# Kernel optimization log

Hardware: AMD Instinct MI355X
Metric: run time of the kernel (lower is better)

Reference implementation:

```python
import jax, jax.numpy as jnp
import numpy as np

T, N, E, F_IN, H_GNN, H_OUT, RH, G, C = 8, 10000, 160000, 128, 128, 128, 128, 32, 10


def gcn_layer(x, src, dst, W, b):
    # PyG GCNConv: h = D^-1/2 (A+I) D^-1/2 (x W) + b, self-loops added, edge weight 1
    h = x @ W  # [N, H]
    ones = jnp.ones((E,), h.dtype)
    deg = jax.ops.segment_sum(ones, dst, num_segments=N) + 1.0  # +1 for self-loop
    dinv = jax.lax.rsqrt(deg)
    coef = dinv[src] * dinv[dst]  # [E]
    agg = jax.ops.segment_sum(h[src] * coef[:, None], dst, num_segments=N)
    agg = agg + h * (dinv * dinv)[:, None]  # self-loop term
    return agg + b


def snapshot_encode(x, edge_index, batch, W1, b1, W2, b2):
    src, dst = edge_index[0], edge_index[1]
    h = jax.nn.relu(gcn_layer(x, src, dst, W1, b1))
    h = jax.nn.relu(gcn_layer(h, src, dst, W2, b2))
    sums = jax.ops.segment_sum(h, batch, num_segments=G)  # global_mean_pool
    cnts = jax.ops.segment_sum(jnp.ones((N,), h.dtype), batch, num_segments=G)
    return sums / jnp.maximum(cnts, 1.0)[:, None]  # [G, H_OUT]


def gru_layer(seq, Wih, Whh, bih, bhh):
    # seq: [T, G, in]; torch nn.GRU cell equations
    H = Whh.shape[1]

    def step(h, xt):
        gi = xt @ Wih.T + bih
        gh = h @ Whh.T + bhh
        ir, iz, inn = jnp.split(gi, 3, axis=-1)
        hr, hz, hn = jnp.split(gh, 3, axis=-1)
        r = jax.nn.sigmoid(ir + hr)
        z = jax.nn.sigmoid(iz + hz)
        n = jnp.tanh(inn + r * hn)
        h_new = (1.0 - z) * n + z * h
        return h_new, h_new

    h0 = jnp.zeros((seq.shape[1], H), seq.dtype)
    hT, outs = jax.lax.scan(step, h0, seq)
    return outs, hT


def setup_inputs() -> dict:
    key = jax.random.key(0)
    ks = jax.random.split(key, 20)
    s = 0.05
    inp = {
        "x": jax.random.normal(ks[0], (T, N, F_IN), jnp.float32),
        "edge_index": jax.random.randint(ks[1], (T, 2, E), 0, N),
        "batch": jax.random.randint(ks[2], (T, N), 0, G),
        "W1": jax.random.normal(ks[3], (F_IN, H_GNN), jnp.float32) * s,
        "b1": jnp.zeros((H_GNN,), jnp.float32),
        "W2": jax.random.normal(ks[4], (H_GNN, H_OUT), jnp.float32) * s,
        "b2": jnp.zeros((H_OUT,), jnp.float32),
        "Wih0": jax.random.normal(ks[5], (3 * RH, H_OUT), jnp.float32) * s,
        "Whh0": jax.random.normal(ks[6], (3 * RH, RH), jnp.float32) * s,
        "bih0": jnp.zeros((3 * RH,), jnp.float32),
        "bhh0": jnp.zeros((3 * RH,), jnp.float32),
        "Wih1": jax.random.normal(ks[7], (3 * RH, RH), jnp.float32) * s,
        "Whh1": jax.random.normal(ks[8], (3 * RH, RH), jnp.float32) * s,
        "bih1": jnp.zeros((3 * RH,), jnp.float32),
        "bhh1": jnp.zeros((3 * RH,), jnp.float32),
        "Wc": jax.random.normal(ks[9], (C, RH), jnp.float32) * s,
        "bc": jnp.zeros((C,), jnp.float32),
    }
    return inp


def reference(x, edge_index, batch, W1, b1, W2, b2, Wih0, Whh0, bih0, bhh0,
              Wih1, Whh1, bih1, bhh1, Wc, bc):
    # per-snapshot GNN encode, vmapped over T snapshots -> [T, G, H_OUT]
    emb = jax.vmap(snapshot_encode, in_axes=(0, 0, 0, None, None, None, None))(
        x, edge_index, batch, W1, b1, W2, b2)
    outs, _ = gru_layer(emb, Wih0, Whh0, bih0, bhh0)
    _, hT = gru_layer(outs, Wih1, Whh1, bih1, bhh1)  # h_n[-1]: last layer final state
    return hT @ Wc.T + bc  # [G, C]
```

## Files before the change

kernel.cpp:

```cpp
#include <hip/hip_runtime.h>

#define T_ 8
#define N_ 10000
#define E_ 160000
#define G_ 32
#define C_ 10
#define F_ 128

typedef _Float16 f16;
typedef _Float16 f16x2 __attribute__((ext_vector_type(2)));
typedef _Float16 f16x4 __attribute__((ext_vector_type(4)));
typedef _Float16 f16x8 __attribute__((ext_vector_type(8)));
typedef float floatx4 __attribute__((ext_vector_type(4)));

static constexpr int NSL = 16;
static constexpr int SLICE = E_ / NSL;

static constexpr size_t OFF_XH    = 0;
static constexpr size_t OFF_A1    = 20480000;
static constexpr size_t OFF_H1    = 40960000;
static constexpr size_t OFF_REC   = 61440000;
static constexpr size_t OFF_CNT   = 66560000;
static constexpr size_t OFF_DINV  = 71680000;
static constexpr size_t OFF_RP    = 72000000;
static constexpr size_t OFF_CNTG  = 72320032;
static constexpr size_t OFF_BRP   = 72321056;
static constexpr size_t OFF_WP    = 72322112;
static constexpr size_t OFF_BLIST = 72387648;
static constexpr size_t OFF_GPACK = 72707648;
static constexpr size_t OFF_PART  = 73100864;

__device__ __forceinline__ float sig_fast(float x) {
  return __builtin_amdgcn_rcpf(1.0f + __builtin_amdgcn_exp2f(-1.4426950408889634f * x));
}
__device__ __forceinline__ float tanh_fast(float x) {
  return 1.0f - 2.0f * __builtin_amdgcn_rcpf(1.0f + __builtin_amdgcn_exp2f(2.8853900817779268f * x));
}

__global__ __launch_bounds__(1024) void prep0_kernel(const int* __restrict__ ei,
                                                     const int* __restrict__ batch,
                                                     int* __restrict__ cnt,
                                                     int* __restrict__ cntG,
                                                     const float* __restrict__ W1,
                                                     const float* __restrict__ W2,
                                                     f16* __restrict__ Wp,
                                                     const float* __restrict__ A0,
                                                     const float* __restrict__ A1,
                                                     const float* __restrict__ A2,
                                                     const float* __restrict__ A3,
                                                     f16* __restrict__ gp) {
  __shared__ int hL[N_];
  __shared__ int cL[G_];
  int b = blockIdx.x, tid = threadIdx.x;
  if (b >= 128) {
    int idx = (b - 128) * 1024 + tid;
    if (idx < 32768) {
      const float* W = (idx < 16384) ? W1 : W2;
      int l = idx & 16383;
      int j = l & 7, lane = (l >> 3) & 63, ct = (l >> 9) & 7, kc = (l >> 12) & 3;
      int k = kc * 32 + ((lane >> 4) & 3) * 8 + j;
      int n = ct * 16 + (lane & 15);
      Wp[idx] = (f16)W[k * 128 + n];
    } else {
      int gidx = idx - 32768;
      int mat = gidx / 49152, l = gidx - mat * 49152;
      int j = l & 7, lane = (l >> 3) & 63, kc = (l >> 9) & 3, nt = l >> 11;
      int k = kc * 32 + ((lane >> 4) & 3) * 8 + j;
      int u = nt * 16 + (lane & 15);
      const float* W = (mat == 0) ? A0 : (mat == 1) ? A1 : (mat == 2) ? A2 : A3;
      gp[gidx] = (f16)W[u * 128 + k];
    }
    return;
  }
  int t = b & 7, s = b >> 3;
  for (int i = tid; i < N_; i += 1024) hL[i] = 0;
  if (tid < G_) cL[tid] = 0;
  __syncthreads();
  const int* dstp = ei + (size_t)t * 2 * E_ + E_ + s * SLICE;
  for (int e4 = tid; e4 < SLICE / 4; e4 += 1024) {
    int4 d = *(const int4*)(dstp + e4 * 4);
    atomicAdd(&hL[d.x], 1); atomicAdd(&hL[d.y], 1);
    atomicAdd(&hL[d.z], 1); atomicAdd(&hL[d.w], 1);
  }
  if (s == 0)
    for (int n = tid; n < N_; n += 1024) atomicAdd(&cL[batch[t * N_ + n]], 1);
  __syncthreads();
  int* cp = cnt + ((size_t)t * NSL + s) * N_;
  for (int i = tid; i < N_; i += 1024) cp[i] = hL[i];
  if (s == 0 && tid < G_) cntG[t * G_ + tid] = cL[tid];
}

__global__ __launch_bounds__(1024) void scan_kernel(int* __restrict__ cnt,
                                                    int* __restrict__ rp,
                                                    float* __restrict__ dinv,
                                                    const int* __restrict__ cntG,
                                                    int* __restrict__ brp) {
  __shared__ int wsum[16];
  __shared__ int carry;
  int t = blockIdx.x, tid = threadIdx.x, lane = tid & 63, wid = tid >> 6;
  if (t == 8) {
    int v = (tid < 256) ? cntG[tid] : 0;
    for (int ofs = 1; ofs < 64; ofs <<= 1) {
      int u = __shfl_up(v, ofs);
      if (lane >= ofs) v += u;
    }
    if (lane == 63 && wid < 4) wsum[wid] = v;
    __syncthreads();
    if (tid < 256) {
      int base = 0;
      for (int w = 0; w < wid; ++w) base += wsum[w];
      if (tid == 0) brp[0] = 0;
      brp[tid + 1] = v + base;
    }
    return;
  }
  if (tid == 0) { carry = 0; rp[t * (N_ + 1)] = 0; }
  __syncthreads();
  for (int c0 = 0; c0 < N_; c0 += 1024) {
    int n = c0 + tid;
    int vs[NSL];
    int deg = 0;
    if (n < N_) {
#pragma unroll
      for (int s = 0; s < NSL; ++s) {
        vs[s] = cnt[((size_t)t * NSL + s) * N_ + n];
        deg += vs[s];
      }
      dinv[t * N_ + n] = rsqrtf((float)deg + 1.0f);
    }
    int v = (n < N_) ? deg : 0;
    int v0 = v;
    for (int ofs = 1; ofs < 64; ofs <<= 1) {
      int u = __shfl_up(v, ofs);
      if (lane >= ofs) v += u;
    }
    if (lane == 63) wsum[wid] = v;
    __syncthreads();
    if (wid == 0) {
      int w = (lane < 16) ? wsum[lane] : 0;
      for (int ofs = 1; ofs < 16; ofs <<= 1) {
        int u = __shfl_up(w, ofs);
        if (lane >= ofs) w += u;
      }
      if (lane < 16) wsum[lane] = w;
    }
    __syncthreads();
    int base = carry + (wid ? wsum[wid - 1] : 0);
    if (n < N_) {
      rp[t * (N_ + 1) + n + 1] = base + v;
      int run = base + v - v0;
#pragma unroll
      for (int s = 0; s < NSL; ++s) {
        int vv = vs[s];
        cnt[((size_t)t * NSL + s) * N_ + n] = run;
        run += vv;
      }
    }
    __syncthreads();
    if (tid == 0) carry += wsum[15];
    __syncthreads();
  }
}

__global__ __launch_bounds__(1024) void cvtfill_kernel(const int* __restrict__ ei,
                                                       const int* __restrict__ base,
                                                       int* __restrict__ rec,
                                                       const int* __restrict__ batch,
                                                       const int* __restrict__ brp,
                                                       int* __restrict__ blist,
                                                       const float* __restrict__ x,
                                                       const float* __restrict__ dinv,
                                                       f16* __restrict__ xh) {
  __shared__ int offL[N_];
  __shared__ int cb[G_];
  int b = blockIdx.x, tid = threadIdx.x;
  if (b >= 128) {
    size_t i = ((size_t)(b - 128) * 1024 + tid) * 4;
    float4 v = *(const float4*)(x + i);
    float d = dinv[i >> 7];
    f16x4 o; o.x = (f16)(v.x * d); o.y = (f16)(v.y * d);
    o.z = (f16)(v.z * d); o.w = (f16)(v.w * d);
    *(f16x4*)(xh + i) = o;
    return;
  }
  int t = b & 7, s = b >> 3;
  const int* bp = base + ((size_t)t * NSL + s) * N_;
  for (int i = tid; i < N_; i += 1024) offL[i] = bp[i];
  if (s == 0 && tid < G_) cb[tid] = brp[t * G_ + tid];
  __syncthreads();
  const int* srcp = ei + (size_t)t * 2 * E_ + s * SLICE;
  const int* dstp = srcp + E_;
  int* rt = rec + (size_t)t * E_;
  for (int e4 = tid; e4 < SLICE / 4; e4 += 1024) {
    int4 sv = *(const int4*)(srcp + e4 * 4);
    int4 dv = *(const int4*)(dstp + e4 * 4);
    int p0 = atomicAdd(&offL[dv.x], 1);
    int p1 = atomicAdd(&offL[dv.y], 1);
    int p2 = atomicAdd(&offL[dv.z], 1);
    int p3 = atomicAdd(&offL[dv.w], 1);
    rt[p0] = sv.x; rt[p1] = sv.y; rt[p2] = sv.z; rt[p3] = sv.w;
  }
  if (s == 0) {
    for (int n = tid; n < N_; n += 1024) {
      int g = batch[t * N_ + n];
      int p = atomicAdd(&cb[g], 1);
      blist[p] = t * N_ + n;
    }
  }
}

__global__ __launch_bounds__(256) void agg_kernel(const f16* __restrict__ X, f16* __restrict__ A,
                                                  const int* __restrict__ rp,
                                                  const int* __restrict__ rec,
                                                  const float* __restrict__ dinv) {
  int wave = threadIdx.x >> 6, lane = threadIdx.x & 63;
  int eg = lane >> 4;
  int cb = (lane & 15) * 8;
  int b = blockIdx.x;
  int t = b & 7, i = b >> 3;
  int n = i * 4 + wave;
  int row = t * N_ + n;
  float ds = dinv[row];
  int beg = rp[t * (N_ + 1) + n], end = rp[t * (N_ + 1) + n + 1];
  beg = __builtin_amdgcn_readfirstlane(beg);
  end = __builtin_amdgcn_readfirstlane(end);
  const int* rcb = rec + (size_t)t * E_ + beg + eg;
  const f16* Xt = X + (size_t)t * N_ * F_;

  float s[8] = {0.f, 0.f, 0.f, 0.f, 0.f, 0.f, 0.f, 0.f};
  if (eg == 3) {
    f16x8 v = *(const f16x8*)(Xt + (size_t)n * F_ + cb);
#pragma unroll
    for (int j = 0; j < 8; ++j) s[j] += (float)v[j];
  }
  int cnt = end - beg;
  int nq = cnt >> 2;
  if (nq > 0) {
    int rid0 = rcb[0];
    int rid1 = (nq > 1) ? rcb[4] : 0;
    int rid2 = (nq > 2) ? rcb[8] : 0;
    f16x8 vA = *(const f16x8*)(Xt + (size_t)rid0 * F_ + cb);
    f16x8 vB, vC;
    if (nq > 1) vB = *(const f16x8*)(Xt + (size_t)rid1 * F_ + cb);
    if (nq > 2) vC = *(const f16x8*)(Xt + (size_t)rid2 * F_ + cb);
    int ridN = (nq > 3) ? rcb[12] : 0;
    for (int q = 0; q + 3 < nq; ++q) {
      f16x8 vD = *(const f16x8*)(Xt + (size_t)ridN * F_ + cb);
      int ridNN = rcb[(q + 4) * 4];
#pragma unroll
      for (int j = 0; j < 8; ++j) s[j] += (float)vA[j];
      vA = vB; vB = vC; vC = vD; ridN = ridNN;
    }
#pragma unroll
    for (int j = 0; j < 8; ++j) s[j] += (float)vA[j];
    if (nq > 1) {
#pragma unroll
      for (int j = 0; j < 8; ++j) s[j] += (float)vB[j];
    }
    if (nq > 2) {
#pragma unroll
      for (int j = 0; j < 8; ++j) s[j] += (float)vC[j];
    }
  }
  int rem = cnt & 3;
  if (eg < rem) {
    int rid = rcb[nq * 4];
    f16x8 v = *(const f16x8*)(Xt + (size_t)rid * F_ + cb);
#pragma unroll
    for (int j = 0; j < 8; ++j) s[j] += (float)v[j];
  }
#pragma unroll
  for (int j = 0; j < 8; ++j) {
    s[j] += __shfl_xor(s[j], 16);
    s[j] += __shfl_xor(s[j], 32);
  }
  if (eg == 0) {
    f16x8 o;
#pragma unroll
    for (int j = 0; j < 8; ++j) o[j] = (f16)(ds * s[j]);
    *(f16x8*)(A + (size_t)row * F_ + cb) = o;
  }
}

__global__ __launch_bounds__(256) void gemm_kernel(const f16* __restrict__ A,
                                                   const f16* __restrict__ Wp,
                                                   const float* __restrict__ bias,
                                                   const float* __restrict__ scale,
                                                   f16* __restrict__ O) {
  __shared__ f16x8 Bp[2048];
  const f16x8* Wv = (const f16x8*)Wp;
  for (int i = threadIdx.x; i < 2048; i += 256) Bp[i] = Wv[i];
  __syncthreads();
  int wave = threadIdx.x >> 6, lane = threadIdx.x & 63;
  int quad = lane >> 4, m = lane & 15;
  int rowbase = blockIdx.x * 64 + wave * 16;
  const f16x8* Arow = (const f16x8*)(A + (size_t)(rowbase + m) * F_);
  floatx4 acc[8];
#pragma unroll
  for (int ct = 0; ct < 8; ++ct) { floatx4 z = {0.f, 0.f, 0.f, 0.f}; acc[ct] = z; }
#pragma unroll
  for (int kc = 0; kc < 4; ++kc) {
    f16x8 a = Arow[kc * 4 + quad];
#pragma unroll
    for (int ct = 0; ct < 8; ++ct)
      acc[ct] = __builtin_amdgcn_mfma_f32_16x16x32_f16(a, Bp[(kc * 8 + ct) * 64 + lane],
                                                       acc[ct], 0, 0, 0);
  }
  float sv[4];
#pragma unroll
  for (int r = 0; r < 4; ++r)
    sv[r] = scale ? scale[rowbase + quad * 4 + r] : 1.0f;
#pragma unroll
  for (int ct = 0; ct < 8; ++ct) {
    int colc = ct * 16 + m;
    float bv = bias[colc];
#pragma unroll
    for (int r = 0; r < 4; ++r) {
      int row = rowbase + quad * 4 + r;
      float v = fmaxf(acc[ct][r] + bv, 0.0f) * sv[r];
      O[(size_t)row * F_ + colc] = (f16)v;
    }
  }
}

__global__ void pool1_kernel(const f16* __restrict__ H, const int* __restrict__ brp,
                             const int* __restrict__ blist, float* __restrict__ part) {
  int b = blockIdx.x;
  int wave = threadIdx.x >> 6, lane = threadIdx.x & 63;
  int idx = b >> 1;
  int s = (b & 1) * 4 + wave;
  int beg = brp[idx], end = brp[idx + 1];
  beg = __builtin_amdgcn_readfirstlane(beg);
  end = __builtin_amdgcn_readfirstlane(end);
  int len = end - beg;
  int lo = beg + (int)(((long long)len * s) >> 3);
  int hi = beg + (int)(((long long)len * (s + 1)) >> 3);
  float a00 = 0.f, a01 = 0.f, a10 = 0.f, a11 = 0.f;
  float a20 = 0.f, a21 = 0.f, a30 = 0.f, a31 = 0.f;
  int e = lo;
  for (; e + 3 < hi; e += 4) {
    int r0 = blist[e], r1 = blist[e + 1], r2 = blist[e + 2], r3 = blist[e + 3];
    f16x2 v0 = *(const f16x2*)(H + (size_t)r0 * F_ + 2 * lane);
    f16x2 v1 = *(const f16x2*)(H + (size_t)r1 * F_ + 2 * lane);
    f16x2 v2 = *(const f16x2*)(H + (size_t)r2 * F_ + 2 * lane);
    f16x2 v3 = *(const f16x2*)(H + (size_t)r3 * F_ + 2 * lane);
    a00 += (float)v0.x; a01 += (float)v0.y;
    a10 += (float)v1.x; a11 += (float)v1.y;
    a20 += (float)v2.x; a21 += (float)v2.y;
    a30 += (float)v3.x; a31 += (float)v3.y;
  }
  for (; e < hi; ++e) {
    int r = blist[e];
    f16x2 v = *(const f16x2*)(H + (size_t)r * F_ + 2 * lane);
    a00 += (float)v.x; a01 += (float)v.y;
  }
  float2 o;
  o.x = (a00 + a10) + (a20 + a30);
  o.y = (a01 + a11) + (a21 + a31);
  *(float2*)(part + ((size_t)idx * 8 + s) * F_ + 2 * lane) = o;
}

__global__ __launch_bounds__(256, 1) void gru_mega(
    const f16* __restrict__ gp, const float* __restrict__ part,
    const int* __restrict__ brp,
    const float* __restrict__ bih0, const float* __restrict__ bhh0,
    const float* __restrict__ bih1, const float* __restrict__ bhh1,
    const float* __restrict__ Wc, const float* __restrict__ bc,
    float* __restrict__ out) {
  __shared__ f16 emb_l[16][136];
  __shared__ float gib0[16][384];
  __shared__ f16 hb0[16 * 136];
  __shared__ f16 hb1[16 * 136];
  __shared__ float ghb[2 * 384];
  __shared__ float gib[2 * 384];
  __shared__ float h1s[2 * 128];
  int tid = threadIdx.x, wave = tid >> 6, lane = tid & 63;
  int quad = lane >> 4, mm = lane & 15;
  int g2 = tid >> 7, f = tid & 127;
  int bid = blockIdx.x;

  {
    int r = tid >> 4;
    int fb = (tid & 15) * 8;
    int idx = (r >> 1) * G_ + bid * 2 + (r & 1);
    float s[8] = {0.f, 0.f, 0.f, 0.f, 0.f, 0.f, 0.f, 0.f};
#pragma unroll
    for (int k = 0; k < 8; ++k) {
      const float* p = part + ((size_t)idx * 8 + k) * F_ + fb;
      float4 v0 = *(const float4*)p;
      float4 v1 = *(const float4*)(p + 4);
      s[0] += v0.x; s[1] += v0.y; s[2] += v0.z; s[3] += v0.w;
      s[4] += v1.x; s[5] += v1.y; s[6] += v1.z; s[7] += v1.w;
    }
    float d = fmaxf((float)(brp[idx + 1] - brp[idx]), 1.0f);
    f16x8 ev;
#pragma unroll
    for (int j = 0; j < 8; ++j) ev[j] = (f16)(s[j] / d);
    *(f16x8*)(&emb_l[r][fb]) = ev;
  }
  __syncthreads();

  {
    floatx4 acc[6];
#pragma unroll
    for (int i = 0; i < 6; ++i) { floatx4 z = {0.f, 0.f, 0.f, 0.f}; acc[i] = z; }
#pragma unroll
    for (int kc = 0; kc < 4; ++kc) {
      f16x8 a = *(const f16x8*)(&emb_l[mm][kc * 32 + quad * 8]);
#pragma unroll
      for (int i = 0; i < 6; ++i) {
        int nt = wave * 6 + i;
        f16x8 bf = *(const f16x8*)(gp + (size_t)((nt * 4 + kc) * 64 + lane) * 8);
        acc[i] = __builtin_amdgcn_mfma_f32_16x16x32_f16(a, bf, acc[i], 0, 0, 0);
      }
    }
#pragma unroll
    for (int i = 0; i < 6; ++i)
#pragma unroll
      for (int r = 0; r < 4; ++r)
        gib0[quad * 4 + r][(wave * 6 + i) * 16 + mm] = acc[i][r];
  }

  f16x8 B0[24], B1[24];
#pragma unroll
  for (int i = 0; i < 6; ++i)
#pragma unroll
    for (int kc = 0; kc < 4; ++kc) {
      size_t off = (size_t)((((wave * 6 + i) * 4 + kc) * 64 + lane)) * 8;
      B0[i * 4 + kc] = *(const f16x8*)(gp + 1 * 49152 + off);
      B1[i * 4 + kc] = *(const f16x8*)(gp + 3 * 49152 + off);
    }
  float br0 = bih0[f] + bhh0[f];
  float bz0 = bih0[128 + f] + bhh0[128 + f];
  float bni0 = bih0[256 + f], bnh0 = bhh0[256 + f];
  float br1 = bih1[f] + bhh1[f];
  float bz1 = bih1[128 + f] + bhh1[128 + f];
  float bni1 = bih1[256 + f], bnh1 = bhh1[256 + f];

  for (int i = tid; i < 16 * 136; i += 256) { hb0[i] = (f16)0.f; hb1[i] = (f16)0.f; }
  float h0 = 0.f, h1 = 0.f;
  __syncthreads();

  const f16* wih1 = gp + 2 * 49152;
  for (int t = 0; t < T_; ++t) {
    f16x8 Bs[24];
#pragma unroll
    for (int i = 0; i < 6; ++i)
#pragma unroll
      for (int kc = 0; kc < 4; ++kc)
        Bs[i * 4 + kc] = *(const f16x8*)(wih1 +
            (size_t)((((wave * 6 + i) * 4 + kc) * 64 + lane)) * 8);
    const float* gi = &gib0[t * 2 + g2][0];
    float gir = gi[f], giz = gi[128 + f], gin = gi[256 + f];

    floatx4 acc[6];
#pragma unroll
    for (int i = 0; i < 6; ++i) { floatx4 z = {0.f, 0.f, 0.f, 0.f}; acc[i] = z; }
#pragma unroll
    for (int kc = 0; kc < 4; ++kc) {
      f16x8 a = *(const f16x8*)(hb0 + mm * 136 + kc * 32 + quad * 8);
#pragma unroll
      for (int i = 0; i < 6; ++i)
        acc[i] = __builtin_amdgcn_mfma_f32_16x16x32_f16(a, B0[i * 4 + kc], acc[i], 0, 0, 0);
    }
    if (quad == 0) {
#pragma unroll
      for (int i = 0; i < 6; ++i) {
        ghb[0 * 384 + wave * 96 + i * 16 + mm] = acc[i][0];
        ghb[1 * 384 + wave * 96 + i * 16 + mm] = acc[i][1];
      }
    }
    __syncthreads();

    {
      float hr = ghb[g2 * 384 + f];
      float hz = ghb[g2 * 384 + 128 + f];
      float hn = ghb[g2 * 384 + 256 + f];
      float r = sig_fast(gir + hr + br0);
      float z = sig_fast(giz + hz + bz0);
      float nn = tanh_fast(gin + bni0 + r * (hn + bnh0));
      h0 = (1.0f - z) * nn + z * h0;
      hb0[g2 * 136 + f] = (f16)h0;
    }
    __syncthreads();

    floatx4 accx[6], acch[6];
#pragma unroll
    for (int i = 0; i < 6; ++i) {
      floatx4 z = {0.f, 0.f, 0.f, 0.f}; accx[i] = z; acch[i] = z;
    }
#pragma unroll
    for (int kc = 0; kc < 4; ++kc) {
      f16x8 ax = *(const f16x8*)(hb0 + mm * 136 + kc * 32 + quad * 8);
      f16x8 ah = *(const f16x8*)(hb1 + mm * 136 + kc * 32 + quad * 8);
#pragma unroll
      for (int i = 0; i < 6; ++i) {
        accx[i] = __builtin_amdgcn_mfma_f32_16x16x32_f16(ax, Bs[i * 4 + kc], accx[i], 0, 0, 0);
        acch[i] = __builtin_amdgcn_mfma_f32_16x16x32_f16(ah, B1[i * 4 + kc], acch[i], 0, 0, 0);
      }
    }
    if (quad == 0) {
#pragma unroll
      for (int i = 0; i < 6; ++i) {
        gib[0 * 384 + wave * 96 + i * 16 + mm] = accx[i][0];
        gib[1 * 384 + wave * 96 + i * 16 + mm] = accx[i][1];
        ghb[0 * 384 + wave * 96 + i * 16 + mm] = acch[i][0];
        ghb[1 * 384 + wave * 96 + i * 16 + mm] = acch[i][1];
      }
    }
    __syncthreads();

    {
      float i1r = gib[g2 * 384 + f];
      float i1z = gib[g2 * 384 + 128 + f];
      float i1n = gib[g2 * 384 + 256 + f];
      float hr = ghb[g2 * 384 + f];
      float hz = ghb[g2 * 384 + 128 + f];
      float hn = ghb[g2 * 384 + 256 + f];
      float r = sig_fast(i1r + hr + br1);
      float z = sig_fast(i1z + hz + bz1);
      float nn = tanh_fast(i1n + bni1 + r * (hn + bnh1));
      h1 = (1.0f - z) * nn + z * h1;
      hb1[g2 * 136 + f] = (f16)h1;
    }
    __syncthreads();
  }

  h1s[g2 * 128 + f] = h1;
  __syncthreads();
  if (tid < 2 * C_) {
    int gg = tid / C_, c = tid - gg * C_;
    float s = bc[c];
    const float* wr = Wc + (size_t)c * 128;
    const float* hr = h1s + gg * 128;
    for (int k = 0; k < 128; k += 4) {
      float4 w = *(const float4*)(wr + k);
      s += hr[k] * w.x + hr[k + 1] * w.y + hr[k + 2] * w.z + hr[k + 3] * w.w;
    }
    out[(bid * 2 + gg) * C_ + c] = s;
  }
}

extern "C" void kernel_launch(void* const* d_in, const int* in_sizes, int n_in,
                              void* d_out, int out_size, void* d_ws, size_t ws_size,
                              hipStream_t stream) {
  const float* x    = (const float*)d_in[0];
  const int*   ei   = (const int*)d_in[1];
  const int*   batch= (const int*)d_in[2];
  const float* W1   = (const float*)d_in[3];
  const float* b1   = (const float*)d_in[4];
  const float* W2   = (const float*)d_in[5];
  const float* b2   = (const float*)d_in[6];
  const float* Wih0 = (const float*)d_in[7];
  const float* Whh0 = (const float*)d_in[8];
  const float* bih0 = (const float*)d_in[9];
  const float* bhh0 = (const float*)d_in[10];
  const float* Wih1 = (const float*)d_in[11];
  const float* Whh1 = (const float*)d_in[12];
  const float* bih1 = (const float*)d_in[13];
  const float* bhh1 = (const float*)d_in[14];
  const float* Wc   = (const float*)d_in[15];
  const float* bc   = (const float*)d_in[16];
  float* out = (float*)d_out;

  char* ws = (char*)d_ws;
  f16*   Xh    = (f16*)(ws + OFF_XH);
  f16*   A1    = (f16*)(ws + OFF_A1);
  f16*   H1    = (f16*)(ws + OFF_H1);
  f16*   A2    = A1;
  f16*   H2    = Xh;
  int*   rec   = (int*)(ws + OFF_REC);
  int*   cnt   = (int*)(ws + OFF_CNT);
  float* dinv  = (float*)(ws + OFF_DINV);
  int*   rp    = (int*)(ws + OFF_RP);
  int*   cntG  = (int*)(ws + OFF_CNTG);
  int*   brp   = (int*)(ws + OFF_BRP);
  f16*   Wp    = (f16*)(ws + OFF_WP);
  int*   blist = (int*)(ws + OFF_BLIST);
  f16*   gp    = (f16*)(ws + OFF_GPACK);
  float* part  = (float*)(ws + OFF_PART);

  prep0_kernel<<<352, 1024, 0, stream>>>(ei, batch, cnt, cntG,
                                         W1, W2, Wp, Wih0, Whh0, Wih1, Whh1, gp);
  scan_kernel<<<9, 1024, 0, stream>>>(cnt, rp, dinv, cntG, brp);
  cvtfill_kernel<<<2628, 1024, 0, stream>>>(ei, cnt, rec, batch, brp, blist, x, dinv, Xh);

  agg_kernel<<<20000, 256, 0, stream>>>(Xh, A1, rp, rec, dinv);
  gemm_kernel<<<1250, 256, 0, stream>>>(A1, Wp, b1, dinv, H1);
  agg_kernel<<<20000, 256, 0, stream>>>(H1, A2, rp, rec, dinv);
  gemm_kernel<<<1250, 256, 0, stream>>>(A2, Wp + 16384, b2, (const float*)nullptr, H2);

  pool1_kernel<<<512, 256, 0, stream>>>(H2, brp, blist, part);
  gru_mega<<<16, 256, 0, stream>>>(gp, part, brp, bih0, bhh0, bih1, bhh1, Wc, bc, out);
}
```

Baseline: 283.0 us.

## Reorder GCN to transform-then-aggregate and fuse bias/ReLU into aggregation

Changes each GCN layer from aggregate-then-GEMM to GEMM-then-aggregate. The first GEMM reads fp32 x directly and converts it to f16 in-kernel, which removes the separate x-to-f16 conversion pass from the fill kernel. Bias, ReLU and the dinv scaling move into the aggregation epilogue, so layer 1's source-side dinv is now applied per edge through a gather of dinv[src]. The first GEMM is launched before the scan, so it can start without depending on graph preprocessing. The cost is an extra per-edge scalar load in layer 1 and a GEMM that reads fp32 input.

Result: slower. 295.1 us (+4.3%).

```diff
diff --git a/kernel.cpp b/kernel.cpp
--- a/kernel.cpp
+++ b/kernel.cpp
@@ -16,8 +16,8 @@
 static constexpr int NSL = 16;
 static constexpr int SLICE = E_ / NSL;
 
-static constexpr size_t OFF_XH    = 0;
-static constexpr size_t OFF_A1    = 20480000;
+static constexpr size_t OFF_H2    = 0;
+static constexpr size_t OFF_G     = 20480000;
 static constexpr size_t OFF_H1    = 40960000;
 static constexpr size_t OFF_REC   = 61440000;
 static constexpr size_t OFF_CNT   = 66560000;
@@ -162,27 +162,15 @@
   }
 }
 
-__global__ __launch_bounds__(1024) void cvtfill_kernel(const int* __restrict__ ei,
-                                                       const int* __restrict__ base,
-                                                       int* __restrict__ rec,
-                                                       const int* __restrict__ batch,
-                                                       const int* __restrict__ brp,
-                                                       int* __restrict__ blist,
-                                                       const float* __restrict__ x,
-                                                       const float* __restrict__ dinv,
-                                                       f16* __restrict__ xh) {
+__global__ __launch_bounds__(1024) void fill_kernel(const int* __restrict__ ei,
+                                                    const int* __restrict__ base,
+                                                    int* __restrict__ rec,
+                                                    const int* __restrict__ batch,
+                                                    const int* __restrict__ brp,
+                                                    int* __restrict__ blist) {
   __shared__ int offL[N_];
   __shared__ int cb[G_];
   int b = blockIdx.x, tid = threadIdx.x;
-  if (b >= 128) {
-    size_t i = ((size_t)(b - 128) * 1024 + tid) * 4;
-    float4 v = *(const float4*)(x + i);
-    float d = dinv[i >> 7];
-    f16x4 o; o.x = (f16)(v.x * d); o.y = (f16)(v.y * d);
-    o.z = (f16)(v.z * d); o.w = (f16)(v.w * d);
-    *(f16x4*)(xh + i) = o;
-    return;
-  }
   int t = b & 7, s = b >> 3;
   const int* bp = base + ((size_t)t * NSL + s) * N_;
   for (int i = tid; i < N_; i += 1024) offL[i] = bp[i];
@@ -209,10 +197,52 @@
   }
 }
 
-__global__ __launch_bounds__(256) void agg_kernel(const f16* __restrict__ X, f16* __restrict__ A,
+template <int FP32A>
+__global__ __launch_bounds__(256) void gemm_kernel(const void* __restrict__ Ap,
+                                                   const f16* __restrict__ Wp,
+                                                   f16* __restrict__ O) {
+  __shared__ f16x8 Bp[2048];
+  const f16x8* Wv = (const f16x8*)Wp;
+  for (int i = threadIdx.x; i < 2048; i += 256) Bp[i] = Wv[i];
+  __syncthreads();
+  int wave = threadIdx.x >> 6, lane = threadIdx.x & 63;
+  int quad = lane >> 4, m = lane & 15;
+  int rowbase = blockIdx.x * 64 + wave * 16;
+  floatx4 acc[8];
+#pragma unroll
+  for (int ct = 0; ct < 8; ++ct) { floatx4 z = {0.f, 0.f, 0.f, 0.f}; acc[ct] = z; }
+#pragma unroll
+  for (int kc = 0; kc < 4; ++kc) {
+    f16x8 a;
+    if (FP32A) {
+      const float* Ar = (const float*)Ap + (size_t)(rowbase + m) * F_ + kc * 32 + quad * 8;
+      float4 lo = *(const float4*)Ar;
+      float4 hi = *(const float4*)(Ar + 4);
+      a[0] = (f16)lo.x; a[1] = (f16)lo.y; a[2] = (f16)lo.z; a[3] = (f16)lo.w;
+      a[4] = (f16)hi.x; a[5] = (f16)hi.y; a[6] = (f16)hi.z; a[7] = (f16)hi.w;
+    } else {
+      a = ((const f16x8*)((const f16*)Ap + (size_t)(rowbase + m) * F_))[kc * 4 + quad];
+    }
+#pragma unroll
+    for (int ct = 0; ct < 8; ++ct)
+      acc[ct] = __builtin_amdgcn_mfma_f32_16x16x32_f16(a, Bp[(kc * 8 + ct) * 64 + lane],
+                                                       acc[ct], 0, 0, 0);
+  }
+#pragma unroll
+  for (int ct = 0; ct < 8; ++ct) {
+    int colc = ct * 16 + m;
+#pragma unroll
+    for (int r = 0; r < 4; ++r)
+      O[(size_t)(rowbase + quad * 4 + r) * F_ + colc] = (f16)acc[ct][r];
+  }
+}
+
+template <int L1>
+__global__ __launch_bounds__(256) void agg_kernel(const f16* __restrict__ X, f16* __restrict__ O,
                                                   const int* __restrict__ rp,
                                                   const int* __restrict__ rec,
-                                                  const float* __restrict__ dinv) {
+                                                  const float* __restrict__ dinv,
+                                                  const float* __restrict__ bias) {
   int wave = threadIdx.x >> 6, lane = threadIdx.x & 63;
   int eg = lane >> 4;
   int cb = (lane & 15) * 8;
@@ -226,12 +256,14 @@
   end = __builtin_amdgcn_readfirstlane(end);
   const int* rcb = rec + (size_t)t * E_ + beg + eg;
   const f16* Xt = X + (size_t)t * N_ * F_;
+  const float* dt = dinv + t * N_;
 
   float s[8] = {0.f, 0.f, 0.f, 0.f, 0.f, 0.f, 0.f, 0.f};
   if (eg == 3) {
     f16x8 v = *(const f16x8*)(Xt + (size_t)n * F_ + cb);
-#pragma unroll
-    for (int j = 0; j < 8; ++j) s[j] += (float)v[j];
+    float c = L1 ? ds : 1.0f;
+#pragma unroll
+    for (int j = 0; j < 8; ++j) s[j] += c * (float)v[j];
   }
   int cnt = end - beg;
   int nq = cnt >> 2;
@@ -240,34 +272,38 @@
     int rid1 = (nq > 1) ? rcb[4] : 0;
     int rid2 = (nq > 2) ? rcb[8] : 0;
     f16x8 vA = *(const f16x8*)(Xt + (size_t)rid0 * F_ + cb);
+    float dvA = L1 ? dt[rid0] : 1.0f;
     f16x8 vB, vC;
-    if (nq > 1) vB = *(const f16x8*)(Xt + (size_t)rid1 * F_ + cb);
-    if (nq > 2) vC = *(const f16x8*)(Xt + (size_t)rid2 * F_ + cb);
+    float dvB = 1.0f, dvC = 1.0f;
+    if (nq > 1) { vB = *(const f16x8*)(Xt + (size_t)rid1 * F_ + cb); if (L1) dvB = dt[rid1]; }
+    if (nq > 2) { vC = *(const f16x8*)(Xt + (size_t)rid2 * F_ + cb); if (L1) dvC = dt[rid2]; }
     int ridN = (nq > 3) ? rcb[12] : 0;
     for (int q = 0; q + 3 < nq; ++q) {
       f16x8 vD = *(const f16x8*)(Xt + (size_t)ridN * F_ + cb);
+      float dvD = L1 ? dt[ridN] : 1.0f;
       int ridNN = rcb[(q + 4) * 4];
 #pragma unroll
-      for (int j = 0; j < 8; ++j) s[j] += (float)vA[j];
-      vA = vB; vB = vC; vC = vD; ridN = ridNN;
-    }
-#pragma unroll
-    for (int j = 0; j < 8; ++j) s[j] += (float)vA[j];
+      for (int j = 0; j < 8; ++j) s[j] += L1 ? dvA * (float)vA[j] : (float)vA[j];
+      vA = vB; vB = vC; vC = vD; dvA = dvB; dvB = dvC; dvC = dvD; ridN = ridNN;
+    }
+#pragma unroll
+    for (int j = 0; j < 8; ++j) s[j] += L1 ? dvA * (float)vA[j] : (float)vA[j];
     if (nq > 1) {
 #pragma unroll
-      for (int j = 0; j < 8; ++j) s[j] += (float)vB[j];
+      for (int j = 0; j < 8; ++j) s[j] += L1 ? dvB * (float)vB[j] : (float)vB[j];
     }
     if (nq > 2) {
 #pragma unroll
-      for (int j = 0; j < 8; ++j) s[j] += (float)vC[j];
+      for (int j = 0; j < 8; ++j) s[j] += L1 ? dvC * (float)vC[j] : (float)vC[j];
     }
   }
   int rem = cnt & 3;
   if (eg < rem) {
     int rid = rcb[nq * 4];
     f16x8 v = *(const f16x8*)(Xt + (size_t)rid * F_ + cb);
-#pragma unroll
-    for (int j = 0; j < 8; ++j) s[j] += (float)v[j];
+    float dv = L1 ? dt[rid] : 1.0f;
+#pragma unroll
+    for (int j = 0; j < 8; ++j) s[j] += L1 ? dv * (float)v[j] : (float)v[j];
   }
 #pragma unroll
   for (int j = 0; j < 8; ++j) {
@@ -275,51 +311,17 @@
     s[j] += __shfl_xor(s[j], 32);
   }
   if (eg == 0) {
+    float4 b0 = *(const float4*)(bias + cb);
+    float4 b1v = *(const float4*)(bias + cb + 4);
+    float bb[8] = {b0.x, b0.y, b0.z, b0.w, b1v.x, b1v.y, b1v.z, b1v.w};
     f16x8 o;
 #pragma unroll
-    for (int j = 0; j < 8; ++j) o[j] = (f16)(ds * s[j]);
-    *(f16x8*)(A + (size_t)row * F_ + cb) = o;
-  }
-}
-
-__global__ __launch_bounds__(256) void gemm_kernel(const f16* __restrict__ A,
-                                                   const f16* __restrict__ Wp,
-                                                   const float* __restrict__ bias,
-                                                   const float* __restrict__ scale,
-                                                   f16* __restrict__ O) {
-  __shared__ f16x8 Bp[2048];
-  const f16x8* Wv = (const f16x8*)Wp;
-  for (int i = threadIdx.x; i < 2048; i += 256) Bp[i] = Wv[i];
-  __syncthreads();
-  int wave = threadIdx.x >> 6, lane = threadIdx.x & 63;
-  int quad = lane >> 4, m = lane & 15;
-  int rowbase = blockIdx.x * 64 + wave * 16;
-  const f16x8* Arow = (const f16x8*)(A + (size_t)(rowbase + m) * F_);
-  floatx4 acc[8];
-#pragma unroll
-  for (int ct = 0; ct < 8; ++ct) { floatx4 z = {0.f, 0.f, 0.f, 0.f}; acc[ct] = z; }
-#pragma unroll
-  for (int kc = 0; kc < 4; ++kc) {
-    f16x8 a = Arow[kc * 4 + quad];
-#pragma unroll
-    for (int ct = 0; ct < 8; ++ct)
-      acc[ct] = __builtin_amdgcn_mfma_f32_16x16x32_f16(a, Bp[(kc * 8 + ct) * 64 + lane],
-                                                       acc[ct], 0, 0, 0);
-  }
-  float sv[4];
-#pragma unroll
-  for (int r = 0; r < 4; ++r)
-    sv[r] = scale ? scale[rowbase + quad * 4 + r] : 1.0f;
-#pragma unroll
-  for (int ct = 0; ct < 8; ++ct) {
-    int colc = ct * 16 + m;
-    float bv = bias[colc];
-#pragma unroll
-    for (int r = 0; r < 4; ++r) {
-      int row = rowbase + quad * 4 + r;
-      float v = fmaxf(acc[ct][r] + bv, 0.0f) * sv[r];
-      O[(size_t)row * F_ + colc] = (f16)v;
-    }
+    for (int j = 0; j < 8; ++j) {
+      float v = fmaxf(ds * s[j] + bb[j], 0.0f);
+      if (L1) v *= ds;
+      o[j] = (f16)v;
+    }
+    *(f16x8*)(O + (size_t)row * F_ + cb) = o;
   }
 }
 
@@ -564,11 +566,9 @@
   float* out = (float*)d_out;
 
   char* ws = (char*)d_ws;
-  f16*   Xh    = (f16*)(ws + OFF_XH);
-  f16*   A1    = (f16*)(ws + OFF_A1);
-  f16*   H1    = (f16*)(ws + OFF_H1);
-  f16*   A2    = A1;
-  f16*   H2    = Xh;
+  f16*   H2    = (f16*)(ws + OFF_H2);
+  f16*   G     = (f16*)(ws + OFF_G);
+  f16*   H1p   = (f16*)(ws + OFF_H1);
   int*   rec   = (int*)(ws + OFF_REC);
   int*   cnt   = (int*)(ws + OFF_CNT);
   float* dinv  = (float*)(ws + OFF_DINV);
@@ -582,13 +582,13 @@
 
   prep0_kernel<<<352, 1024, 0, stream>>>(ei, batch, cnt, cntG,
                                          W1, W2, Wp, Wih0, Whh0, Wih1, Whh1, gp);
+  gemm_kernel<1><<<1250, 256, 0, stream>>>(x, Wp, G);
   scan_kernel<<<9, 1024, 0, stream>>>(cnt, rp, dinv, cntG, brp);
-  cvtfill_kernel<<<2628, 1024, 0, stream>>>(ei, cnt, rec, batch, brp, blist, x, dinv, Xh);
-
-  agg_kernel<<<20000, 256, 0, stream>>>(Xh, A1, rp, rec, dinv);
-  gemm_kernel<<<1250, 256, 0, stream>>>(A1, Wp, b1, dinv, H1);
-  agg_kernel<<<20000, 256, 0, stream>>>(H1, A2, rp, rec, dinv);
-  gemm_kernel<<<1250, 256, 0, stream>>>(A2, Wp + 16384, b2, (const float*)nullptr, H2);
+  fill_kernel<<<128, 1024, 0, stream>>>(ei, cnt, rec, batch, brp, blist);
+
+  agg_kernel<1><<<20000, 256, 0, stream>>>(G, H1p, rp, rec, dinv, b1);
+  gemm_kernel<0><<<1250, 256, 0, stream>>>(H1p, Wp + 16384, G);
+  agg_kernel<0><<<20000, 256, 0, stream>>>(G, H2, rp, rec, dinv, b2);
 
   pool1_kernel<<<512, 256, 0, stream>>>(H2, brp, blist, part);
   gru_mega<<<16, 256, 0, stream>>>(gp, part, brp, bih0, bhh0, bih1, bhh1, Wc, bc, out);
```
